# Performance work log

Hardware: AMD Instinct MI355X
Metric: run time of the kernel (lower is better)

## Reference

```python
import jax, jax.numpy as jnp
import numpy as np

B, N, D, K = 8, 4096, 1024, 128
LN_EPS = 1e-5


def _layer_norm(x, g, b):
    m = jnp.mean(x, axis=-1, keepdims=True)
    v = jnp.mean(jnp.square(x - m), axis=-1, keepdims=True)
    return (x - m) * jax.lax.rsqrt(v + LN_EPS) * g + b


def setup_inputs() -> dict:
    key = jax.random.key(0)
    ks = jax.random.split(key, 8)
    # conv init in torch: normal(0, sqrt(2 / (k * out_channels))), k=1
    s_dd = np.sqrt(2.0 / D)  # conv_in, conv_out: out_channels = D
    s_kd = np.sqrt(2.0 / K)  # linear_0: out_channels = K
    s_dk = np.sqrt(2.0 / D)  # linear_1: out_channels = D
    return {
        "x": jax.random.normal(ks[0], (B, N, D), dtype=jnp.float32),
        "ln_g": jnp.ones((D,), jnp.float32),
        "ln_b": jnp.zeros((D,), jnp.float32),
        "w_in": jax.random.normal(ks[1], (D, D), jnp.float32) * s_dd,  # (out, in)
        "b_in": jnp.zeros((D,), jnp.float32),
        "w0": jax.random.normal(ks[2], (K, D), jnp.float32) * s_kd,    # linear_0 (K, D)
        "w1": jax.random.normal(ks[3], (D, K), jnp.float32) * s_dk,    # linear_1 (D, K)
        "w_out": jax.random.normal(ks[4], (D, D), jnp.float32) * s_dd,
        "oln_g": jnp.ones((D,), jnp.float32),
        "oln_b": jnp.zeros((D,), jnp.float32),
    }


def reference(x, ln_g, ln_b, w_in, b_in, w0, w1, w_out, oln_g, oln_b):
    idn = x
    h = _layer_norm(x, ln_g, ln_b)                       # (B, N, D)
    h = jnp.einsum("bnd,ed->bne", h, w_in) + b_in        # conv_in 1x1
    a = jnp.einsum("bnd,kd->bnk", h, w0)                 # (B, N, K)
    a = jax.nn.softmax(a, axis=1)                        # softmax over positions N
    a = a / (1e-9 + jnp.sum(a, axis=2, keepdims=True))   # L1 norm over slots K
    h = jnp.einsum("bnk,dk->bnd", a, w1)                 # linear_1
    h = jnp.einsum("bnd,ed->bne", h, w_out)              # conv_out
    h = _layer_norm(h, oln_g, oln_b)
    return jax.nn.relu(h + idn)
```

## Files before the change

### kernel.cpp

```cpp
#include <hip/hip_runtime.h>
#include <hip/hip_bf16.h>
#include <cstdint>
#include <cstddef>

#define BATCH 8
#define SEQN 4096
#define DIM 1024
#define KSLOT 128
#define MROWS (BATCH * SEQN)
#define LN_EPS 1e-5f

typedef __hip_bfloat16 bf16;
typedef __attribute__((ext_vector_type(8))) short short8;
typedef __attribute__((ext_vector_type(4))) float f32x4;

__device__ __forceinline__ float bf2f(unsigned short u) {
    return __uint_as_float(((unsigned int)u) << 16);
}
__device__ __forceinline__ unsigned short f2bf(float f) {
    unsigned int u = __float_as_uint(f);
    unsigned int r = (u + 0x7fffu + ((u >> 16) & 1u)) >> 16;
    return (unsigned short)r;
}
__device__ __forceinline__ float waveReduceSum(float v) {
    #pragma unroll
    for (int off = 32; off > 0; off >>= 1) v += __shfl_down(v, off, 64);
    return v;
}
__device__ __forceinline__ void load4(const float* p, float* o) {
    float4 v = *reinterpret_cast<const float4*>(p);
    o[0] = v.x; o[1] = v.y; o[2] = v.z; o[3] = v.w;
}
__device__ __forceinline__ void load4(const bf16* p, float* o) {
    ushort4 v = *reinterpret_cast<const ushort4*>(p);
    o[0] = bf2f(v.x); o[1] = bf2f(v.y); o[2] = bf2f(v.z); o[3] = bf2f(v.w);
}
__device__ __forceinline__ void store4(float* p, const float* o) {
    float4 v; v.x = o[0]; v.y = o[1]; v.z = o[2]; v.w = o[3];
    *reinterpret_cast<float4*>(p) = v;
}
__device__ __forceinline__ void store4(bf16* p, const float* o) {
    ushort4 v; v.x = f2bf(o[0]); v.y = f2bf(o[1]); v.z = f2bf(o[2]); v.w = f2bf(o[3]);
    *reinterpret_cast<ushort4*>(p) = v;
}

typedef __attribute__((address_space(1))) const void gvoid;
typedef __attribute__((address_space(3))) void lvoid;
__device__ __forceinline__ void async_cp16(const void* g, void* l) {
    __builtin_amdgcn_global_load_lds((gvoid*)g, (lvoid*)l, 16, 0, 0);
}

__global__ __launch_bounds__(256) void nn_partial(
    const float* __restrict__ A, const float* __restrict__ B,
    float* __restrict__ P, int Ka, int E, int Db)
{
    __shared__ float As[16][68];
    __shared__ float Bs[16][68];
    int tid = threadIdx.x, tx = tid & 15, ty = tid >> 4;
    int k0 = blockIdx.x * 64, d0 = blockIdx.y * 64;
    int chunk = E >> 3, e0 = blockIdx.z * chunk;
    int lr = tid >> 2, lk = (tid & 3) * 4;
    int er = tid >> 4, dc = (tid & 15) * 4;
    float acc[4][4] = {};
    for (int et = 0; et < chunk; et += 16) {
        float av[4], bv[4];
        load4(A + (size_t)(k0 + lr) * E + e0 + et + lk, av);
        load4(B + (size_t)(e0 + et + er) * Db + d0 + dc, bv);
        #pragma unroll
        for (int j = 0; j < 4; j++) { As[lk + j][lr] = av[j]; Bs[er][dc + j] = bv[j]; }
        __syncthreads();
        #pragma unroll
        for (int kk = 0; kk < 16; kk++) {
            float a_[4], b_[4];
            #pragma unroll
            for (int i = 0; i < 4; i++) { a_[i] = As[kk][ty * 4 + i]; b_[i] = Bs[kk][tx * 4 + i]; }
            #pragma unroll
            for (int i = 0; i < 4; i++)
                #pragma unroll
                for (int j = 0; j < 4; j++) acc[i][j] += a_[i] * b_[j];
        }
        __syncthreads();
    }
    float* base = P + ((size_t)blockIdx.z * Ka + k0) * Db + d0;
    #pragma unroll
    for (int i = 0; i < 4; i++) store4(base + (size_t)(ty * 4 + i) * Db + tx * 4, acc[i]);
}

__global__ __launch_bounds__(256) void reduce_split8(
    const float* __restrict__ P1, const float* __restrict__ P2,
    bf16* __restrict__ hi1, bf16* __restrict__ lo1,
    bf16* __restrict__ hi2, bf16* __restrict__ lo2, int n)
{
    int bid = blockIdx.x;
    const float* P; bf16 *hi, *lo; int base;
    if (bid < 128) { P = P1; hi = hi1; lo = lo1; base = bid; }
    else           { P = P2; hi = hi2; lo = lo2; base = bid - 128; }
    int i = (base * 256 + threadIdx.x) * 4;
    if (i >= n) return;
    float s[4] = {0.f, 0.f, 0.f, 0.f};
    #pragma unroll
    for (int z = 0; z < 8; z++) {
        float t[4];
        load4(P + (size_t)z * n + i, t);
        #pragma unroll
        for (int j = 0; j < 4; j++) s[j] += t[j];
    }
    ushort4 h, l;
    unsigned short hb[4], lb[4];
    #pragma unroll
    for (int j = 0; j < 4; j++) {
        hb[j] = f2bf(s[j]);
        lb[j] = f2bf(s[j] - bf2f(hb[j]));
    }
    h.x = hb[0]; h.y = hb[1]; h.z = hb[2]; h.w = hb[3];
    l.x = lb[0]; l.y = lb[1]; l.z = lb[2]; l.w = lb[3];
    reinterpret_cast<ushort4*>(hi)[i >> 2] = h;
    reinterpret_cast<ushort4*>(lo)[i >> 2] = l;
}

__global__ __launch_bounds__(64) void bias_comb(
    const float* __restrict__ w0, const float* __restrict__ b_in, float* __restrict__ bias0)
{
    int k = blockIdx.x, lane = threadIdx.x;
    float s = 0.0f;
    for (int e = lane; e < DIM; e += 64) s += w0[(size_t)k * DIM + e] * b_in[e];
    s = waveReduceSum(s);
    if (lane == 0) bias0[k] = s;
}

__global__ __launch_bounds__(256) void ln_in_kernel(
    const float* __restrict__ x, const float* __restrict__ g,
    const float* __restrict__ b, bf16* __restrict__ out)
{
    int r = blockIdx.x;
    int t = threadIdx.x;
    float v[4];
    load4(x + (size_t)r * DIM + t * 4, v);
    float sum = v[0] + v[1] + v[2] + v[3];
    float sq  = v[0]*v[0] + v[1]*v[1] + v[2]*v[2] + v[3]*v[3];
    sum = waveReduceSum(sum);
    sq  = waveReduceSum(sq);
    __shared__ float sA[4], sB[4];
    __shared__ float mean_s, rstd_s;
    int w = t >> 6;
    if ((t & 63) == 0) { sA[w] = sum; sB[w] = sq; }
    __syncthreads();
    if (t == 0) {
        float S = sA[0] + sA[1] + sA[2] + sA[3];
        float Q = sB[0] + sB[1] + sB[2] + sB[3];
        float mean = S * (1.0f / DIM);
        float var = Q * (1.0f / DIM) - mean * mean;
        mean_s = mean;
        rstd_s = rsqrtf(fmaxf(var, 0.0f) + LN_EPS);
    }
    __syncthreads();
    float mean = mean_s, rstd = rstd_s;
    float gv[4], bv[4], o[4];
    load4(g + t * 4, gv);
    load4(b + t * 4, bv);
    #pragma unroll
    for (int j = 0; j < 4; j++) o[j] = (v[j] - mean) * rstd * gv[j] + bv[j];
    store4(out + (size_t)r * DIM + t * 4, o);
}

__global__ __launch_bounds__(256) void gemm_logits(
    const bf16* __restrict__ A, const bf16* __restrict__ Whi, const bf16* __restrict__ Wlo,
    const float* __restrict__ bias, float* __restrict__ C, int M, int Kin)
{
    __shared__ short As[64 * 32];
    __shared__ short Wh[128 * 32];
    __shared__ short Wl[128 * 32];
    const int tid = threadIdx.x, wave = tid >> 6, lane = tid & 63;
    const int wm = wave >> 1, wn = wave & 1;
    const int m0 = blockIdx.x * 64;
    const int srow = tid >> 2, scol = (tid & 3) * 8;
    const bf16* aG  = A   + (size_t)(m0 + srow) * Kin + scol;
    const bf16* hG0 = Whi + (size_t)srow * Kin + scol;
    const bf16* hG1 = hG0 + (size_t)64 * Kin;
    const bf16* lG0 = Wlo + (size_t)srow * Kin + scol;
    const bf16* lG1 = lG0 + (size_t)64 * Kin;
    short* aL  = As + tid * 8;
    short* hL0 = Wh + tid * 8;  short* hL1 = Wh + 2048 + tid * 8;
    short* lL0 = Wl + tid * 8;  short* lL1 = Wl + 2048 + tid * 8;
    const int fr = lane & 15, kb = (lane >> 4) * 8;

    f32x4 acc[2][4];
    #pragma unroll
    for (int i = 0; i < 2; i++)
        #pragma unroll
        for (int j = 0; j < 4; j++) acc[i][j] = 0.0f;

    for (int kt = 0; kt < Kin; kt += 32) {
        async_cp16(aG + kt, aL);
        async_cp16(hG0 + kt, hL0);
        async_cp16(hG1 + kt, hL1);
        async_cp16(lG0 + kt, lL0);
        async_cp16(lG1 + kt, lL1);
        __syncthreads();
        short8 af[2], bh[4], bl[4];
        #pragma unroll
        for (int i = 0; i < 2; i++)
            af[i] = *(const short8*)(As + (wm * 32 + i * 16 + fr) * 32 + kb);
        #pragma unroll
        for (int j = 0; j < 4; j++) {
            bh[j] = *(const short8*)(Wh + (wn * 64 + j * 16 + fr) * 32 + kb);
            bl[j] = *(const short8*)(Wl + (wn * 64 + j * 16 + fr) * 32 + kb);
        }
        #pragma unroll
        for (int i = 0; i < 2; i++)
            #pragma unroll
            for (int j = 0; j < 4; j++) {
                acc[i][j] = __builtin_amdgcn_mfma_f32_16x16x32_bf16(af[i], bh[j], acc[i][j], 0, 0, 0);
                acc[i][j] = __builtin_amdgcn_mfma_f32_16x16x32_bf16(af[i], bl[j], acc[i][j], 0, 0, 0);
            }
        __syncthreads();
    }

    const int crow = (lane >> 4) * 4;
    #pragma unroll
    for (int j = 0; j < 4; j++) {
        int col = wn * 64 + j * 16 + fr;
        float bv = bias[col];
        #pragma unroll
        for (int i = 0; i < 2; i++) {
            int rbase = m0 + wm * 32 + i * 16 + crow;
            #pragma unroll
            for (int r = 0; r < 4; r++)
                C[(size_t)(rbase + r) * KSLOT + col] = acc[i][j][r] + bv;
        }
    }
}

__global__ __launch_bounds__(256) void smax_part_kernel(
    const float* __restrict__ logits, float* __restrict__ pm, float* __restrict__ ps)
{
    int kb = blockIdx.x, nb = blockIdx.y, b = blockIdx.z;
    int tx = threadIdx.x, ty = threadIdx.y;
    int k = kb * 64 + tx;
    const float* base = logits + ((size_t)b * SEQN) * KSLOT + k;
    int n0 = nb * 256 + ty * 64;
    float m = -1e30f, s = 0.0f;
    for (int j = 0; j < 64; j++) {
        float v = base[(size_t)(n0 + j) * KSLOT];
        if (v > m) { s = s * __expf(m - v) + 1.0f; m = v; }
        else       { s += __expf(v - m); }
    }
    __shared__ float lm[4][64], ls[4][64];
    lm[ty][tx] = m; ls[ty][tx] = s;
    __syncthreads();
    if (ty == 0) {
        #pragma unroll
        for (int q = 1; q < 4; q++) {
            float m2 = lm[q][tx], s2 = ls[q][tx];
            float nm = fmaxf(m, m2);
            s = s * __expf(m - nm) + s2 * __expf(m2 - nm);
            m = nm;
        }
        int col = b * KSLOT + k;
        pm[col * 16 + nb] = m;
        ps[col * 16 + nb] = s;
    }
}

__global__ __launch_bounds__(256) void smax_comb_kernel(
    const float* __restrict__ pm, const float* __restrict__ ps,
    float* __restrict__ cm, float* __restrict__ cs)
{
    int c = blockIdx.x * 256 + threadIdx.x;
    float m = -1e30f, s = 0.0f;
    #pragma unroll
    for (int nb = 0; nb < 16; nb++) {
        float m2 = pm[c * 16 + nb], s2 = ps[c * 16 + nb];
        float nm = fmaxf(m, m2);
        s = s * __expf(m - nm) + s2 * __expf(m2 - nm);
        m = nm;
    }
    cm[c] = m;
    cs[c] = s;
}

__global__ __launch_bounds__(512, 4) void h3_fused(
    const float* __restrict__ logits, const float* __restrict__ cm, const float* __restrict__ cs,
    const bf16* __restrict__ Whi, const bf16* __restrict__ Wlo,
    const float* __restrict__ x, const float* __restrict__ g, const float* __restrict__ bb,
    float* __restrict__ out)
{
    __shared__ short As[32 * 128];
    __shared__ float redS[8][32];
    __shared__ float redQ[8][32];
    __shared__ float mrowM[32], mrowR[32];

    const int tid  = threadIdx.x;
    const int wave = tid >> 6, lane = tid & 63;
    const int fr = lane & 15, gq = lane >> 4;
    const int r0 = blockIdx.x * 32;
    const int bIdx = r0 >> 12;

    {
        int row = tid >> 4;
        int c0  = (tid & 15) * 8;
        const float* lp = logits + (size_t)(r0 + row) * KSLOT + c0;
        float v[8], cmv[8], csv[8];
        load4(lp, v);                 load4(lp + 4, v + 4);
        const float* cmp = cm + bIdx * KSLOT + c0;
        const float* csp = cs + bIdx * KSLOT + c0;
        load4(cmp, cmv);              load4(cmp + 4, cmv + 4);
        load4(csp, csv);              load4(csp + 4, csv + 4);
        float e[8], s = 0.0f;
        #pragma unroll
        for (int j = 0; j < 8; j++) { e[j] = __expf(v[j] - cmv[j]) / csv[j]; s += e[j]; }
        #pragma unroll
        for (int off = 1; off < 16; off <<= 1) s += __shfl_xor(s, off, 64);
        float inv = 1.0f / (1e-9f + s);
        short8 pk;
        #pragma unroll
        for (int j = 0; j < 8; j++) pk[j] = (short)f2bf(e[j] * inv);
        int csw = c0 ^ ((row & 7) << 3);
        *(short8*)(As + row * 128 + csw) = pk;
    }
    __syncthreads();

    const int cbase = wave * 128;
    const int kb = gq * 8;
    f32x4 acc[2][8];
    #pragma unroll
    for (int i = 0; i < 2; i++)
        #pragma unroll
        for (int j = 0; j < 8; j++) acc[i][j] = 0.0f;

    for (int kt = 0; kt < KSLOT; kt += 32) {
        short8 af[2];
        #pragma unroll
        for (int i = 0; i < 2; i++) {
            int row = i * 16 + fr;
            af[i] = *(const short8*)(As + row * 128 + ((kt + kb) ^ ((row & 7) << 3)));
        }
        #pragma unroll
        for (int jc = 0; jc < 4; jc++) {
            short8 bh[2], bl[2];
            #pragma unroll
            for (int j = 0; j < 2; j++) {
                int d = cbase + (jc * 2 + j) * 16 + fr;
                bh[j] = *(const short8*)((const short*)Whi + (size_t)d * KSLOT + kt + kb);
                bl[j] = *(const short8*)((const short*)Wlo + (size_t)d * KSLOT + kt + kb);
            }
            #pragma unroll
            for (int j = 0; j < 2; j++)
                #pragma unroll
                for (int i = 0; i < 2; i++) {
                    acc[i][jc * 2 + j] = __builtin_amdgcn_mfma_f32_16x16x32_bf16(bh[j], af[i], acc[i][jc * 2 + j], 0, 0, 0);
                    acc[i][jc * 2 + j] = __builtin_amdgcn_mfma_f32_16x16x32_bf16(bl[j], af[i], acc[i][jc * 2 + j], 0, 0, 0);
                }
        }
    }

    {
        #pragma unroll
        for (int i = 0; i < 2; i++) {
            float s = 0.0f, q = 0.0f;
            #pragma unroll
            for (int j = 0; j < 8; j++)
                #pragma unroll
                for (int r = 0; r < 4; r++) {
                    float v = acc[i][j][r];
                    s += v; q += v * v;
                }
            s += __shfl_xor(s, 16, 64);  q += __shfl_xor(q, 16, 64);
            s += __shfl_xor(s, 32, 64);  q += __shfl_xor(q, 32, 64);
            if (gq == 0) { redS[wave][i * 16 + fr] = s; redQ[wave][i * 16 + fr] = q; }
        }
    }
    __syncthreads();
    if (tid < 32) {
        float S = 0.0f, Q = 0.0f;
        #pragma unroll
        for (int w = 0; w < 8; w++) { S += redS[w][tid]; Q += redQ[w][tid]; }
        float mean = S * (1.0f / DIM);
        float var  = Q * (1.0f / DIM) - mean * mean;
        mrowM[tid] = mean;
        mrowR[tid] = rsqrtf(fmaxf(var, 0.0f) + LN_EPS);
    }
    __syncthreads();

    {
        #pragma unroll
        for (int i = 0; i < 2; i++) {
            int row = i * 16 + fr;
            float mean = mrowM[row], rstd = mrowR[row];
            const float* xr = x   + (size_t)(r0 + row) * DIM;
            float*       orow = out + (size_t)(r0 + row) * DIM;
            #pragma unroll
            for (int j = 0; j < 8; j++) {
                int d = cbase + j * 16 + gq * 4;
                float gv[4], bv[4], xv[4], o[4];
                load4(g + d, gv);
                load4(bb + d, bv);
                load4(xr + d, xv);
                #pragma unroll
                for (int r = 0; r < 4; r++) {
                    float z = (acc[i][j][r] - mean) * rstd * gv[r] + bv[r] + xv[r];
                    o[r] = fmaxf(z, 0.0f);
                }
                store4(orow + d, o);
            }
        }
    }
}

extern "C" void kernel_launch(void* const* d_in, const int* in_sizes, int n_in,
                              void* d_out, int out_size, void* d_ws, size_t ws_size,
                              hipStream_t stream)
{
    const float* x     = (const float*)d_in[0];
    const float* ln_g  = (const float*)d_in[1];
    const float* ln_b  = (const float*)d_in[2];
    const float* w_in  = (const float*)d_in[3];
    const float* b_in  = (const float*)d_in[4];
    const float* w0    = (const float*)d_in[5];
    const float* w1    = (const float*)d_in[6];
    const float* w_out = (const float*)d_in[7];
    const float* oln_g = (const float*)d_in[8];
    const float* oln_b = (const float*)d_in[9];
    float* out = (float*)d_out;

    char* ws = (char*)d_ws;
    bf16*  hln    = (bf16*)ws;
    float* logits = (float*)(ws + 67108864);
    float* P1     = (float*)(ws + 67108864);
    float* P2     = (float*)(ws + 71303168);
    bf16*  wc_hi  = (bf16*)(ws + 83886080);
    bf16*  wc_lo  = (bf16*)(ws + 84148224);
    bf16*  wc2_hi = (bf16*)(ws + 84410368);
    bf16*  wc2_lo = (bf16*)(ws + 84672512);
    float* bias0  = (float*)(ws + 84934656);
    float* pm     = (float*)(ws + 84935168);
    float* psum   = (float*)(ws + 85000704);
    float* cm     = (float*)(ws + 85066240);
    float* cs     = (float*)(ws + 85070336);

    nn_partial<<<dim3(2, 16, 8), dim3(256), 0, stream>>>(w0, w_in, P1, KSLOT, DIM, DIM);
    nn_partial<<<dim3(16, 2, 8), dim3(256), 0, stream>>>(w_out, w1, P2, DIM, DIM, KSLOT);
    reduce_split8<<<dim3(256), dim3(256), 0, stream>>>(P1, P2, wc_hi, wc_lo, wc2_hi, wc2_lo, KSLOT * DIM);
    bias_comb<<<dim3(KSLOT), dim3(64), 0, stream>>>(w0, b_in, bias0);
    ln_in_kernel<<<dim3(MROWS), dim3(256), 0, stream>>>(x, ln_g, ln_b, hln);
    gemm_logits<<<dim3(MROWS / 64), dim3(256), 0, stream>>>(
        hln, wc_hi, wc_lo, bias0, logits, MROWS, DIM);
    smax_part_kernel<<<dim3(KSLOT / 64, 16, BATCH), dim3(64, 4), 0, stream>>>(logits, pm, psum);
    smax_comb_kernel<<<dim3(4), dim3(256), 0, stream>>>(pm, psum, cm, cs);
    h3_fused<<<dim3(MROWS / 32), dim3(512), 0, stream>>>(
        logits, cm, cs, wc2_hi, wc2_lo, x, oln_g, oln_b, out);
}
```

Before: 457.1 us.

## Fold input LayerNorm into logits GEMM via gamma-scaled weights and row stats

Drops the separate input LayerNorm pass and its bf16 intermediate buffer. The logits GEMM now reads fp32 x directly, casts it to bf16 on the fly while accumulating row sum and sum of squares, and applies the normalization algebraically in the epilogue using precomputed u = W·g and v = W·b vectors. This removes a full read/write round trip of the activation. The softmax partial kernel is rewritten to use coalesced float4 row reads, h3_fused's inner B-fragment grouping is changed from 2 to 4, and its min-blocks launch bound is dropped. The risk is precision: x is quantized to bf16 before normalization rather than after, which may cost accuracy.

```diff
diff --git a/kernel.cpp b/kernel.cpp
--- a/kernel.cpp
+++ b/kernel.cpp
@@ -31,17 +31,9 @@
     float4 v = *reinterpret_cast<const float4*>(p);
     o[0] = v.x; o[1] = v.y; o[2] = v.z; o[3] = v.w;
 }
-__device__ __forceinline__ void load4(const bf16* p, float* o) {
-    ushort4 v = *reinterpret_cast<const ushort4*>(p);
-    o[0] = bf2f(v.x); o[1] = bf2f(v.y); o[2] = bf2f(v.z); o[3] = bf2f(v.w);
-}
 __device__ __forceinline__ void store4(float* p, const float* o) {
     float4 v; v.x = o[0]; v.y = o[1]; v.z = o[2]; v.w = o[3];
     *reinterpret_cast<float4*>(p) = v;
-}
-__device__ __forceinline__ void store4(bf16* p, const float* o) {
-    ushort4 v; v.x = f2bf(o[0]); v.y = f2bf(o[1]); v.z = f2bf(o[2]); v.w = f2bf(o[3]);
-    *reinterpret_cast<ushort4*>(p) = v;
 }
 
 typedef __attribute__((address_space(1))) const void gvoid;
@@ -86,16 +78,55 @@
     for (int i = 0; i < 4; i++) store4(base + (size_t)(ty * 4 + i) * Db + tx * 4, acc[i]);
 }
 
-__global__ __launch_bounds__(256) void reduce_split8(
-    const float* __restrict__ P1, const float* __restrict__ P2,
-    bf16* __restrict__ hi1, bf16* __restrict__ lo1,
-    bf16* __restrict__ hi2, bf16* __restrict__ lo2, int n)
-{
-    int bid = blockIdx.x;
-    const float* P; bf16 *hi, *lo; int base;
-    if (bid < 128) { P = P1; hi = hi1; lo = lo1; base = bid; }
-    else           { P = P2; hi = hi2; lo = lo2; base = bid - 128; }
-    int i = (base * 256 + threadIdx.x) * 4;
+__global__ __launch_bounds__(256) void w1_prep(
+    const float* __restrict__ P1, const float* __restrict__ g, const float* __restrict__ lb,
+    bf16* __restrict__ hi, bf16* __restrict__ lo,
+    float* __restrict__ u, float* __restrict__ v)
+{
+    int k = blockIdx.x, tid = threadIdx.x;
+    int d = tid * 4;
+    float wcf[4] = {0.f, 0.f, 0.f, 0.f};
+    #pragma unroll
+    for (int z = 0; z < 8; z++) {
+        float t[4];
+        load4(P1 + ((size_t)z * KSLOT + k) * DIM + d, t);
+        #pragma unroll
+        for (int j = 0; j < 4; j++) wcf[j] += t[j];
+    }
+    float gv[4], bv[4];
+    load4(g + d, gv);
+    load4(lb + d, bv);
+    float su = 0.f, sv = 0.f;
+    ushort4 h, l;
+    unsigned short hb[4], lbv[4];
+    #pragma unroll
+    for (int j = 0; j < 4; j++) {
+        float wg = wcf[j] * gv[j];
+        hb[j] = f2bf(wg);
+        lbv[j] = f2bf(wg - bf2f(hb[j]));
+        su += wg;
+        sv += wcf[j] * bv[j];
+    }
+    h.x = hb[0]; h.y = hb[1]; h.z = hb[2]; h.w = hb[3];
+    l.x = lbv[0]; l.y = lbv[1]; l.z = lbv[2]; l.w = lbv[3];
+    reinterpret_cast<ushort4*>(hi)[((size_t)k * DIM + d) >> 2] = h;
+    reinterpret_cast<ushort4*>(lo)[((size_t)k * DIM + d) >> 2] = l;
+    su = waveReduceSum(su);
+    sv = waveReduceSum(sv);
+    __shared__ float sU[4], sV[4];
+    int w = tid >> 6;
+    if ((tid & 63) == 0) { sU[w] = su; sV[w] = sv; }
+    __syncthreads();
+    if (tid == 0) {
+        u[k] = sU[0] + sU[1] + sU[2] + sU[3];
+        v[k] = sV[0] + sV[1] + sV[2] + sV[3];
+    }
+}
+
+__global__ __launch_bounds__(256) void w2_split(
+    const float* __restrict__ P, bf16* __restrict__ hi, bf16* __restrict__ lo, int n)
+{
+    int i = (blockIdx.x * 256 + threadIdx.x) * 4;
     if (i >= n) return;
     float s[4] = {0.f, 0.f, 0.f, 0.f};
     #pragma unroll
@@ -128,60 +159,26 @@
     if (lane == 0) bias0[k] = s;
 }
 
-__global__ __launch_bounds__(256) void ln_in_kernel(
-    const float* __restrict__ x, const float* __restrict__ g,
-    const float* __restrict__ b, bf16* __restrict__ out)
-{
-    int r = blockIdx.x;
-    int t = threadIdx.x;
-    float v[4];
-    load4(x + (size_t)r * DIM + t * 4, v);
-    float sum = v[0] + v[1] + v[2] + v[3];
-    float sq  = v[0]*v[0] + v[1]*v[1] + v[2]*v[2] + v[3]*v[3];
-    sum = waveReduceSum(sum);
-    sq  = waveReduceSum(sq);
-    __shared__ float sA[4], sB[4];
-    __shared__ float mean_s, rstd_s;
-    int w = t >> 6;
-    if ((t & 63) == 0) { sA[w] = sum; sB[w] = sq; }
-    __syncthreads();
-    if (t == 0) {
-        float S = sA[0] + sA[1] + sA[2] + sA[3];
-        float Q = sB[0] + sB[1] + sB[2] + sB[3];
-        float mean = S * (1.0f / DIM);
-        float var = Q * (1.0f / DIM) - mean * mean;
-        mean_s = mean;
-        rstd_s = rsqrtf(fmaxf(var, 0.0f) + LN_EPS);
-    }
-    __syncthreads();
-    float mean = mean_s, rstd = rstd_s;
-    float gv[4], bv[4], o[4];
-    load4(g + t * 4, gv);
-    load4(b + t * 4, bv);
-    #pragma unroll
-    for (int j = 0; j < 4; j++) o[j] = (v[j] - mean) * rstd * gv[j] + bv[j];
-    store4(out + (size_t)r * DIM + t * 4, o);
-}
-
-__global__ __launch_bounds__(256) void gemm_logits(
-    const bf16* __restrict__ A, const bf16* __restrict__ Whi, const bf16* __restrict__ Wlo,
-    const float* __restrict__ bias, float* __restrict__ C, int M, int Kin)
+__global__ __launch_bounds__(256) void gemm_logits_fused(
+    const float* __restrict__ x, const bf16* __restrict__ Whi, const bf16* __restrict__ Wlo,
+    const float* __restrict__ u, const float* __restrict__ v, const float* __restrict__ bias0,
+    float* __restrict__ C)
 {
     __shared__ short As[64 * 32];
     __shared__ short Wh[128 * 32];
     __shared__ short Wl[128 * 32];
+    __shared__ float rowM[64], rowR[64];
     const int tid = threadIdx.x, wave = tid >> 6, lane = tid & 63;
     const int wm = wave >> 1, wn = wave & 1;
     const int m0 = blockIdx.x * 64;
     const int srow = tid >> 2, scol = (tid & 3) * 8;
-    const bf16* aG  = A   + (size_t)(m0 + srow) * Kin + scol;
-    const bf16* hG0 = Whi + (size_t)srow * Kin + scol;
-    const bf16* hG1 = hG0 + (size_t)64 * Kin;
-    const bf16* lG0 = Wlo + (size_t)srow * Kin + scol;
-    const bf16* lG1 = lG0 + (size_t)64 * Kin;
-    short* aL  = As + tid * 8;
+    const bf16* hG0 = Whi + (size_t)srow * DIM + scol;
+    const bf16* hG1 = hG0 + (size_t)64 * DIM;
+    const bf16* lG0 = Wlo + (size_t)srow * DIM + scol;
+    const bf16* lG1 = lG0 + (size_t)64 * DIM;
     short* hL0 = Wh + tid * 8;  short* hL1 = Wh + 2048 + tid * 8;
     short* lL0 = Wl + tid * 8;  short* lL1 = Wl + 2048 + tid * 8;
+    const float* xG = x + (size_t)(m0 + srow) * DIM + scol;
     const int fr = lane & 15, kb = (lane >> 4) * 8;
 
     f32x4 acc[2][4];
@@ -190,12 +187,24 @@
         #pragma unroll
         for (int j = 0; j < 4; j++) acc[i][j] = 0.0f;
 
-    for (int kt = 0; kt < Kin; kt += 32) {
-        async_cp16(aG + kt, aL);
+    float s_acc = 0.0f, q_acc = 0.0f;
+
+    for (int kt = 0; kt < DIM; kt += 32) {
         async_cp16(hG0 + kt, hL0);
         async_cp16(hG1 + kt, hL1);
         async_cp16(lG0 + kt, lL0);
         async_cp16(lG1 + kt, lL1);
+        float xv[8];
+        load4(xG + kt, xv);
+        load4(xG + kt + 4, xv + 4);
+        short8 pk;
+        #pragma unroll
+        for (int j = 0; j < 8; j++) {
+            pk[j] = (short)f2bf(xv[j]);
+            s_acc += xv[j];
+            q_acc += xv[j] * xv[j];
+        }
+        *(short8*)(As + srow * 32 + scol) = pk;
         __syncthreads();
         short8 af[2], bh[4], bl[4];
         #pragma unroll
@@ -216,49 +225,70 @@
         __syncthreads();
     }
 
+    s_acc += __shfl_xor(s_acc, 1, 64);  q_acc += __shfl_xor(q_acc, 1, 64);
+    s_acc += __shfl_xor(s_acc, 2, 64);  q_acc += __shfl_xor(q_acc, 2, 64);
+    if ((tid & 3) == 0) {
+        float mean = s_acc * (1.0f / DIM);
+        float var  = q_acc * (1.0f / DIM) - mean * mean;
+        rowM[srow] = mean;
+        rowR[srow] = rsqrtf(fmaxf(var, 0.0f) + LN_EPS);
+    }
+    __syncthreads();
+
     const int crow = (lane >> 4) * 4;
     #pragma unroll
     for (int j = 0; j < 4; j++) {
         int col = wn * 64 + j * 16 + fr;
-        float bv = bias[col];
+        float uc = u[col];
+        float vc = v[col] + bias0[col];
         #pragma unroll
         for (int i = 0; i < 2; i++) {
-            int rbase = m0 + wm * 32 + i * 16 + crow;
-            #pragma unroll
-            for (int r = 0; r < 4; r++)
-                C[(size_t)(rbase + r) * KSLOT + col] = acc[i][j][r] + bv;
-        }
-    }
-}
-
-__global__ __launch_bounds__(256) void smax_part_kernel(
+            int rl0 = wm * 32 + i * 16 + crow;
+            #pragma unroll
+            for (int r = 0; r < 4; r++) {
+                int rl = rl0 + r;
+                float rstd = rowR[rl], mean = rowM[rl];
+                C[(size_t)(m0 + rl) * KSLOT + col] = rstd * acc[i][j][r] - rstd * mean * uc + vc;
+            }
+        }
+    }
+}
+
+__global__ __launch_bounds__(256) void smax_part_c(
     const float* __restrict__ logits, float* __restrict__ pm, float* __restrict__ ps)
 {
-    int kb = blockIdx.x, nb = blockIdx.y, b = blockIdx.z;
-    int tx = threadIdx.x, ty = threadIdx.y;
-    int k = kb * 64 + tx;
-    const float* base = logits + ((size_t)b * SEQN) * KSLOT + k;
-    int n0 = nb * 256 + ty * 64;
-    float m = -1e30f, s = 0.0f;
-    for (int j = 0; j < 64; j++) {
-        float v = base[(size_t)(n0 + j) * KSLOT];
-        if (v > m) { s = s * __expf(m - v) + 1.0f; m = v; }
-        else       { s += __expf(v - m); }
-    }
-    __shared__ float lm[4][64], ls[4][64];
-    lm[ty][tx] = m; ls[ty][tx] = s;
-    __syncthreads();
-    if (ty == 0) {
-        #pragma unroll
-        for (int q = 1; q < 4; q++) {
-            float m2 = lm[q][tx], s2 = ls[q][tx];
-            float nm = fmaxf(m, m2);
-            s = s * __expf(m - nm) + s2 * __expf(m2 - nm);
-            m = nm;
-        }
-        int col = b * KSLOT + k;
-        pm[col * 16 + nb] = m;
-        ps[col * 16 + nb] = s;
+    int nb = blockIdx.x, b = blockIdx.y;
+    int t = threadIdx.x;
+    int kq = (t & 31) * 4, rg = t >> 5;
+    const float* base = logits + ((size_t)(b * SEQN + nb * 256 + rg)) * KSLOT + kq;
+    float m[4] = {-1e30f, -1e30f, -1e30f, -1e30f};
+    float s[4] = {0.f, 0.f, 0.f, 0.f};
+    for (int it = 0; it < 32; it++) {
+        float vv[4];
+        load4(base + (size_t)it * 8 * KSLOT, vv);
+        #pragma unroll
+        for (int j = 0; j < 4; j++) {
+            float vj = vv[j];
+            if (vj > m[j]) { s[j] = s[j] * __expf(m[j] - vj) + 1.0f; m[j] = vj; }
+            else           { s[j] += __expf(vj - m[j]); }
+        }
+    }
+    __shared__ float lm[8][128], ls[8][128];
+    #pragma unroll
+    for (int j = 0; j < 4; j++) { lm[rg][kq + j] = m[j]; ls[rg][kq + j] = s[j]; }
+    __syncthreads();
+    if (t < 128) {
+        float M = -1e30f, S = 0.f;
+        #pragma unroll
+        for (int r2 = 0; r2 < 8; r2++) {
+            float m2 = lm[r2][t], s2 = ls[r2][t];
+            float nm = fmaxf(M, m2);
+            S = S * __expf(M - nm) + s2 * __expf(m2 - nm);
+            M = nm;
+        }
+        int col = b * KSLOT + t;
+        pm[col * 16 + nb] = M;
+        ps[col * 16 + nb] = S;
     }
 }
 
@@ -279,7 +309,7 @@
     cs[c] = s;
 }
 
-__global__ __launch_bounds__(512, 4) void h3_fused(
+__global__ __launch_bounds__(512) void h3_fused(
     const float* __restrict__ logits, const float* __restrict__ cm, const float* __restrict__ cs,
     const bf16* __restrict__ Whi, const bf16* __restrict__ Wlo,
     const float* __restrict__ x, const float* __restrict__ g, const float* __restrict__ bb,
@@ -336,20 +366,20 @@
             af[i] = *(const short8*)(As + row * 128 + ((kt + kb) ^ ((row & 7) << 3)));
         }
         #pragma unroll
-        for (int jc = 0; jc < 4; jc++) {
-            short8 bh[2], bl[2];
-            #pragma unroll
-            for (int j = 0; j < 2; j++) {
-                int d = cbase + (jc * 2 + j) * 16 + fr;
+        for (int jc = 0; jc < 2; jc++) {
+            short8 bh[4], bl[4];
+            #pragma unroll
+            for (int j = 0; j < 4; j++) {
+                int d = cbase + (jc * 4 + j) * 16 + fr;
                 bh[j] = *(const short8*)((const short*)Whi + (size_t)d * KSLOT + kt + kb);
                 bl[j] = *(const short8*)((const short*)Wlo + (size_t)d * KSLOT + kt + kb);
             }
             #pragma unroll
-            for (int j = 0; j < 2; j++)
+            for (int j = 0; j < 4; j++)
                 #pragma unroll
                 for (int i = 0; i < 2; i++) {
-                    acc[i][jc * 2 + j] = __builtin_amdgcn_mfma_f32_16x16x32_bf16(bh[j], af[i], acc[i][jc * 2 + j], 0, 0, 0);
-                    acc[i][jc * 2 + j] = __builtin_amdgcn_mfma_f32_16x16x32_bf16(bl[j], af[i], acc[i][jc * 2 + j], 0, 0, 0);
+                    acc[i][jc * 4 + j] = __builtin_amdgcn_mfma_f32_16x16x32_bf16(bh[j], af[i], acc[i][jc * 4 + j], 0, 0, 0);
+                    acc[i][jc * 4 + j] = __builtin_amdgcn_mfma_f32_16x16x32_bf16(bl[j], af[i], acc[i][jc * 4 + j], 0, 0, 0);
                 }
         }
     }
@@ -424,7 +454,6 @@
     float* out = (float*)d_out;
 
     char* ws = (char*)d_ws;
-    bf16*  hln    = (bf16*)ws;
     float* logits = (float*)(ws + 67108864);
     float* P1     = (float*)(ws + 67108864);
     float* P2     = (float*)(ws + 71303168);
@@ -437,15 +466,17 @@
     float* psum   = (float*)(ws + 85000704);
     float* cm     = (float*)(ws + 85066240);
     float* cs     = (float*)(ws + 85070336);
+    float* uvec   = (float*)(ws + 85074432);
+    float* vvec   = (float*)(ws + 85078528);
 
     nn_partial<<<dim3(2, 16, 8), dim3(256), 0, stream>>>(w0, w_in, P1, KSLOT, DIM, DIM);
     nn_partial<<<dim3(16, 2, 8), dim3(256), 0, stream>>>(w_out, w1, P2, DIM, DIM, KSLOT);
-    reduce_split8<<<dim3(256), dim3(256), 0, stream>>>(P1, P2, wc_hi, wc_lo, wc2_hi, wc2_lo, KSLOT * DIM);
     bias_comb<<<dim3(KSLOT), dim3(64), 0, stream>>>(w0, b_in, bias0);
-    ln_in_kernel<<<dim3(MROWS), dim3(256), 0, stream>>>(x, ln_g, ln_b, hln);
-    gemm_logits<<<dim3(MROWS / 64), dim3(256), 0, stream>>>(
-        hln, wc_hi, wc_lo, bias0, logits, MROWS, DIM);
-    smax_part_kernel<<<dim3(KSLOT / 64, 16, BATCH), dim3(64, 4), 0, stream>>>(logits, pm, psum);
+    w1_prep<<<dim3(KSLOT), dim3(256), 0, stream>>>(P1, ln_g, ln_b, wc_hi, wc_lo, uvec, vvec);
+    w2_split<<<dim3(128), dim3(256), 0, stream>>>(P2, wc2_hi, wc2_lo, KSLOT * DIM);
+    gemm_logits_fused<<<dim3(MROWS / 64), dim3(256), 0, stream>>>(
+        x, wc_hi, wc_lo, uvec, vvec, bias0, logits);
+    smax_part_c<<<dim3(16, BATCH), dim3(256), 0, stream>>>(logits, pm, psum);
     smax_comb_kernel<<<dim3(4), dim3(256), 0, stream>>>(pm, psum, cm, cs);
     h3_fused<<<dim3(MROWS / 32), dim3(512), 0, stream>>>(
         logits, cm, cs, wc2_hi, wc2_lo, x, oln_g, oln_b, out);
```

Result: faster. 423.2 us (-7.4%).
